# Kernel tuning notes

Measured on AMD Instinct MI355X. Metric: run time of the kernel, lower is better.

Reference implementation:

```python
import jax, jax.numpy as jnp
import numpy as np

N_NODES = 100000
N_EDGES = 1_600_000
IN_DIM, HID, OUT_DIM, N_BLOCKS = 963, 192, 3, 6


def spmm(src, dst, w, x):
    # sparse adj @ x, adj[dst, src] = w  (COO edge list)
    msgs = x[src] * w[:, None]                      # [E, F]
    return jax.ops.segment_sum(msgs, dst, num_segments=N_NODES)


def gconv(x, src, dst, ew, w, lw, b):
    # Pixel2Mesh GConv: adj @ (x @ W) + x @ W_loop + b
    return spmm(src, dst, ew, x @ w) + x @ lw + b


def setup_inputs() -> dict:
    key = jax.random.key(0)
    ks = jax.random.split(key, 13)
    s = 0.02  # small init scale to keep deep stack numerically tame
    return {
        "inputs": jax.random.normal(ks[0], (N_NODES, IN_DIM), jnp.float32),
        "edge_src": jax.random.randint(ks[1], (N_EDGES,), 0, N_NODES),
        "edge_dst": jax.random.randint(ks[2], (N_EDGES,), 0, N_NODES),
        "edge_weight": jax.random.uniform(ks[3], (N_EDGES,), jnp.float32) / 16.0,
        "w_in": jax.random.normal(ks[4], (IN_DIM, HID), jnp.float32) * s,
        "loop_in": jax.random.normal(ks[5], (IN_DIM, HID), jnp.float32) * s,
        "b_in": jnp.zeros((HID,), jnp.float32),
        "blocks_w": jax.random.normal(ks[6], (N_BLOCKS, 2, HID, HID), jnp.float32) * s,
        "blocks_loop": jax.random.normal(ks[7], (N_BLOCKS, 2, HID, HID), jnp.float32) * s,
        "blocks_b": jnp.zeros((N_BLOCKS, 2, HID), jnp.float32),
        "w_out": jax.random.normal(ks[8], (HID, OUT_DIM), jnp.float32) * s,
        "loop_out": jax.random.normal(ks[9], (HID, OUT_DIM), jnp.float32) * s,
        "b_out": jnp.zeros((OUT_DIM,), jnp.float32),
    }


def reference(inputs, edge_src, edge_dst, edge_weight, w_in, loop_in, b_in,
              blocks_w, blocks_loop, blocks_b, w_out, loop_out, b_out):
    x = gconv(inputs, edge_src, edge_dst, edge_weight, w_in, loop_in, b_in)

    def block(x, params):
        bw, bl, bb = params
        h = gconv(x, edge_src, edge_dst, edge_weight, bw[0], bl[0], bb[0])
        h = gconv(h, edge_src, edge_dst, edge_weight, bw[1], bl[1], bb[1])
        return (x + h) * 0.5, None

    x_cat, _ = jax.lax.scan(block, x, (blocks_w, blocks_loop, blocks_b))
    x_out = gconv(x_cat, edge_src, edge_dst, edge_weight, w_out, loop_out, b_out)
    return (x_out, x_cat)
```

## Files before the change

### kernel.cpp

```cpp
#include <hip/hip_runtime.h>
#include <cstdint>
#include <cstddef>

#define N_NODES 100000
#define N_EDGES 1600000
#define IN_DIM 963
#define HID 192
#define OUT_DIM 3

typedef _Float16 f16x8 __attribute__((ext_vector_type(8)));
typedef float f32x4 __attribute__((ext_vector_type(4)));

__global__ void count_kernel(const int* __restrict__ dst, int* __restrict__ counts, int E) {
    int i = blockIdx.x * blockDim.x + threadIdx.x;
    if (i < E) atomicAdd(&counts[dst[i]], 1);
}

__global__ __launch_bounds__(256)
void scan_local(const int* __restrict__ counts, int* __restrict__ rp,
                int* __restrict__ bsum, int n) {
    __shared__ int sm[256];
    const int base = blockIdx.x * 1024;
    const int t = threadIdx.x;
    const int i0 = base + t * 4;
    int v[4];
#pragma unroll
    for (int j = 0; j < 4; ++j) v[j] = (i0 + j < n) ? counts[i0 + j] : 0;
    v[1] += v[0]; v[2] += v[1]; v[3] += v[2];
    sm[t] = v[3];
    __syncthreads();
    for (int off = 1; off < 256; off <<= 1) {
        int add = (t >= off) ? sm[t - off] : 0;
        __syncthreads();
        sm[t] += add;
        __syncthreads();
    }
    const int pre = (t > 0) ? sm[t - 1] : 0;
#pragma unroll
    for (int j = 0; j < 4; ++j) {
        int idx = i0 + j;
        if (idx < n) rp[idx + 1] = pre + v[j];
    }
    if (t == 255) bsum[blockIdx.x] = sm[255];
}

__global__ __launch_bounds__(128)
void scan_block(int* __restrict__ bsum, int nb) {
    __shared__ int sm[128];
    const int t = threadIdx.x;
    const int v = (t < nb) ? bsum[t] : 0;
    sm[t] = v;
    __syncthreads();
    for (int off = 1; off < 128; off <<= 1) {
        int add = (t >= off) ? sm[t - off] : 0;
        __syncthreads();
        sm[t] += add;
        __syncthreads();
    }
    if (t < nb) bsum[t] = sm[t] - v;
}

__global__ void scan_add(const int* __restrict__ bsum, int* __restrict__ rp, int n) {
    int i = blockIdx.x * blockDim.x + threadIdx.x;
    if (i < n) rp[i + 1] += bsum[i >> 10];
    if (i == 0) rp[0] = 0;
}

__global__ void copy_cursor_kernel(const int* __restrict__ rp, int* __restrict__ cursor, int n) {
    int i = blockIdx.x * blockDim.x + threadIdx.x;
    if (i < n) cursor[i] = rp[i];
}

__global__ void scatter_kernel(const int* __restrict__ src, const int* __restrict__ dst,
                               const float* __restrict__ w, int* __restrict__ cursor,
                               int* __restrict__ csr_src, float* __restrict__ csr_w,
                               int* __restrict__ csr_eid, int E) {
    int i = blockIdx.x * blockDim.x + threadIdx.x;
    if (i < E) {
        int d = dst[i];
        int p = atomicAdd(&cursor[d], 1);
        csr_src[p] = src[i];
        csr_w[p] = w[i];
        csr_eid[p] = i;
    }
}

__global__ void sortrow_kernel(const int* __restrict__ rp, int* __restrict__ csr_src,
                               float* __restrict__ csr_w, int* __restrict__ csr_eid, int n) {
    int r = blockIdx.x * blockDim.x + threadIdx.x;
    if (r >= n) return;
    int s = rp[r], e = rp[r + 1];
    for (int i = s + 1; i < e; ++i) {
        int ke = csr_eid[i]; int ks = csr_src[i]; float kw = csr_w[i];
        int j = i - 1;
        while (j >= s && csr_eid[j] > ke) {
            csr_eid[j + 1] = csr_eid[j];
            csr_src[j + 1] = csr_src[j];
            csr_w[j + 1] = csr_w[j];
            --j;
        }
        csr_eid[j + 1] = ke; csr_src[j + 1] = ks; csr_w[j + 1] = kw;
    }
}

__global__ __launch_bounds__(256)
void trans_split(const float* __restrict__ W, const float* __restrict__ L,
                 int K, int Kp, _Float16* __restrict__ out_hi, _Float16* __restrict__ out_lo) {
    __shared__ float tile[32][33];
    const int n0 = blockIdx.x * 32, k0 = blockIdx.y * 32;
    const int tx = threadIdx.x, ty = threadIdx.y;
#pragma unroll
    for (int i = 0; i < 4; ++i) {
        int k = k0 + ty + i * 8;
        int n = n0 + tx;
        float v = 0.f;
        if (k < K) v = (n < HID) ? W[(size_t)k * HID + n] : L[(size_t)k * HID + (n - HID)];
        tile[ty + i * 8][tx] = v;
    }
    __syncthreads();
#pragma unroll
    for (int i = 0; i < 4; ++i) {
        int nl = ty + i * 8;
        int n = n0 + nl;
        int k = k0 + tx;
        float v = tile[tx][nl];
        _Float16 hi = (_Float16)v;
        _Float16 lo = (_Float16)(v - (float)hi);
        out_hi[(size_t)n * Kp + k] = hi;
        out_lo[(size_t)n * Kp + k] = lo;
    }
}

__global__ __launch_bounds__(256, 2)
void gemm_lds(const float* __restrict__ X, int M, int Kx, int Kp,
              const _Float16* __restrict__ Wth, const _Float16* __restrict__ Wtl,
              const float* __restrict__ bias, const float* __restrict__ res,
              float* __restrict__ Hdst, float* __restrict__ Tdst) {
    __shared__ __align__(16) char smem[81920];

    const int m0 = blockIdx.x * 128;
    const int tid = threadIdx.x;
    const int lane = tid & 63;
    const int wave = tid >> 6;
    const int wr = wave >> 1;
    const int wc = wave & 1;
    const int kg = lane >> 4;
    const int bcol = blockIdx.y * 192;

    auto stage = [&](int k0, int cb) {
#pragma unroll
        for (int i = 0; i < 4; ++i) {
            const int id = i * 256 + tid;
            const int row = id >> 3, slot = id & 7;
            int gr = m0 + row; if (gr >= M) gr = 0;
            const int srck = k0 + ((slot ^ (row & 7)) << 2);
            const float* src = X + (size_t)gr * Kx + srck;
            void* dst = (void*)(smem + cb + (i * 256 + wave * 64) * 16);
            __builtin_amdgcn_global_load_lds(
                (const __attribute__((address_space(1))) void*)src,
                (__attribute__((address_space(3))) void*)dst, 16, 0, 0);
        }
#pragma unroll
        for (int i = 0; i < 3; ++i) {
            const int id = i * 256 + tid;
            const int row = id >> 2, slot = id & 3;
            const int srck = k0 + ((slot ^ ((row >> 1) & 3)) << 3);
            const size_t go = (size_t)(bcol + row) * Kp + srck;
            void* dsth = (void*)(smem + cb + 16384 + (i * 256 + wave * 64) * 16);
            void* dstl = (void*)(smem + cb + 28672 + (i * 256 + wave * 64) * 16);
            __builtin_amdgcn_global_load_lds(
                (const __attribute__((address_space(1))) void*)(Wth + go),
                (__attribute__((address_space(3))) void*)dsth, 16, 0, 0);
            __builtin_amdgcn_global_load_lds(
                (const __attribute__((address_space(1))) void*)(Wtl + go),
                (__attribute__((address_space(3))) void*)dstl, 16, 0, 0);
        }
    };

    f32x4 acc[4][6];
#pragma unroll
    for (int i = 0; i < 4; ++i)
#pragma unroll
        for (int j = 0; j < 6; ++j)
            acc[i][j] = f32x4{0.f, 0.f, 0.f, 0.f};

    const int nsteps = (Kx + 31) / 32;

    stage(0, 0);
    __syncthreads();

    for (int s = 0; s < nsteps; ++s) {
        const int cb = (s & 1) * 40960;
        if (s + 1 < nsteps) stage((s + 1) * 32, ((s + 1) & 1) * 40960);

        const char* cur = smem + cb;
        f16x8 fah[4], fal[4];
#pragma unroll
        for (int mi = 0; mi < 4; ++mi) {
            const int row = wr * 64 + mi * 16 + (lane & 15);
            const char* rb = cur + row * 128;
            f32x4 a0 = *(const f32x4*)(rb + ((((2 * kg)     ^ (row & 7))) << 4));
            f32x4 a1 = *(const f32x4*)(rb + ((((2 * kg + 1) ^ (row & 7))) << 4));
            f16x8 hi, lo;
#pragma unroll
            for (int j = 0; j < 4; ++j) {
                float x0 = a0[j], x1 = a1[j];
                _Float16 h0 = (_Float16)x0, h1 = (_Float16)x1;
                hi[j] = h0;     hi[4 + j] = h1;
                lo[j] = (_Float16)(x0 - (float)h0);
                lo[4 + j] = (_Float16)(x1 - (float)h1);
            }
            fah[mi] = hi; fal[mi] = lo;
        }
#pragma unroll
        for (int ni = 0; ni < 6; ++ni) {
            const int idx = wc * 96 + ni * 16 + (lane & 15);
            const int off = 16384 + idx * 64 + ((kg ^ ((idx >> 1) & 3)) << 4);
            const f16x8 fbh = *(const f16x8*)(cur + off);
            const f16x8 fbl = *(const f16x8*)(cur + off + 12288);
#pragma unroll
            for (int mi = 0; mi < 4; ++mi)
                acc[mi][ni] = __builtin_amdgcn_mfma_f32_16x16x32_f16(fah[mi], fbh, acc[mi][ni], 0, 0, 0);
#pragma unroll
            for (int mi = 0; mi < 4; ++mi)
                acc[mi][ni] = __builtin_amdgcn_mfma_f32_16x16x32_f16(fal[mi], fbh, acc[mi][ni], 0, 0, 0);
#pragma unroll
            for (int mi = 0; mi < 4; ++mi)
                acc[mi][ni] = __builtin_amdgcn_mfma_f32_16x16x32_f16(fah[mi], fbl, acc[mi][ni], 0, 0, 0);
        }
        __syncthreads();
    }

    const bool isH = (bcol == 0);
#pragma unroll
    for (int mi = 0; mi < 4; ++mi) {
        const int rbase = m0 + wr * 64 + mi * 16 + ((lane >> 4) << 2);
#pragma unroll
        for (int ni = 0; ni < 6; ++ni) {
            const int gc = wc * 96 + ni * 16 + (lane & 15);
            f32x4 v = acc[mi][ni];
            if (isH) {
#pragma unroll
                for (int j = 0; j < 4; ++j) {
                    const int row = rbase + j;
                    if (row < M) Hdst[(size_t)row * HID + gc] = v[j];
                }
            } else {
                const float bv = bias[gc];
#pragma unroll
                for (int j = 0; j < 4; ++j) {
                    const int row = rbase + j;
                    if (row < M) {
                        float t = v[j] + bv;
                        if (res != nullptr) t += res[(size_t)row * HID + gc];
                        Tdst[(size_t)row * HID + gc] = t;
                    }
                }
            }
        }
    }
}

__global__ __launch_bounds__(256, 4)
void spmm_kernel(const int* __restrict__ rp, const int* __restrict__ csrc,
                 const float* __restrict__ cw, const float* __restrict__ Hm,
                 float* __restrict__ out, float scale) {
    const int lane = threadIdx.x & 63;
    const int nwaves = (gridDim.x * blockDim.x) >> 6;
    const int ntasks = N_NODES * 3;
    for (int task = (blockIdx.x * blockDim.x + threadIdx.x) >> 6; task < ntasks;
         task += nwaves) {
        const int wid = task / 3;
        const int ch = task - wid * 3;
        const int s = __builtin_amdgcn_readfirstlane(rp[wid]);
        const int e = __builtin_amdgcn_readfirstlane(rp[wid + 1]);
        const int fo = ch * 64 + lane;
        float a = 0.f;
        int i = s;
        for (; i + 15 < e; i += 16) {
            float w[16], x[16];
#pragma unroll
            for (int u = 0; u < 16; ++u) {
                w[u] = cw[i + u];
                x[u] = Hm[(size_t)csrc[i + u] * HID + fo];
            }
#pragma unroll
            for (int u = 0; u < 16; ++u) a += w[u] * x[u];
        }
        for (; i + 3 < e; i += 4) {
            float w[4], x[4];
#pragma unroll
            for (int u = 0; u < 4; ++u) {
                w[u] = cw[i + u];
                x[u] = Hm[(size_t)csrc[i + u] * HID + fo];
            }
#pragma unroll
            for (int u = 0; u < 4; ++u) a += w[u] * x[u];
        }
        for (; i < e; ++i)
            a += cw[i] * Hm[(size_t)csrc[i] * HID + fo];
        float* o = out + (size_t)wid * HID + ch * 64;
        o[lane] = scale * (o[lane] + a);
    }
}

__global__ __launch_bounds__(256)
void out_gemm(const float* __restrict__ X, const float* __restrict__ Wout,
              const float* __restrict__ Lout, const float* __restrict__ bout,
              float* __restrict__ H3, float* __restrict__ T3) {
    __shared__ float Ws[HID * OUT_DIM];
    __shared__ float Ls[HID * OUT_DIM];
    int tid = threadIdx.x;
    for (int i = tid; i < HID * OUT_DIM; i += 256) { Ws[i] = Wout[i]; Ls[i] = Lout[i]; }
    __syncthreads();
    int n = blockIdx.x * 4 + (tid >> 6);
    int lane = tid & 63;
    if (n >= N_NODES) return;
    const float* x = X + (size_t)n * HID;
    float aw[3] = {0.f, 0.f, 0.f}, al[3] = {0.f, 0.f, 0.f};
#pragma unroll
    for (int p = 0; p < 3; ++p) {
        int k = p * 64 + lane;
        float xv = x[k];
#pragma unroll
        for (int c = 0; c < 3; ++c) {
            aw[c] += xv * Ws[k * 3 + c];
            al[c] += xv * Ls[k * 3 + c];
        }
    }
#pragma unroll
    for (int off = 32; off > 0; off >>= 1) {
#pragma unroll
        for (int c = 0; c < 3; ++c) {
            aw[c] += __shfl_down(aw[c], off, 64);
            al[c] += __shfl_down(al[c], off, 64);
        }
    }
    if (lane == 0) {
#pragma unroll
        for (int c = 0; c < 3; ++c) {
            H3[n * 3 + c] = aw[c];
            T3[n * 3 + c] = al[c] + bout[c];
        }
    }
}

__global__ __launch_bounds__(256)
void out_spmm(const int* __restrict__ rp, const int* __restrict__ csrc,
              const float* __restrict__ cw, const float* __restrict__ H3,
              const float* __restrict__ T3, float* __restrict__ out) {
    int n = blockIdx.x * blockDim.x + threadIdx.x;
    if (n >= N_NODES) return;
    int s = rp[n], e = rp[n + 1];
    float a0 = 0.f, a1 = 0.f, a2 = 0.f;
    for (int i = s; i < e; ++i) {
        float w = cw[i];
        int src = csrc[i];
        a0 += w * H3[src * 3 + 0];
        a1 += w * H3[src * 3 + 1];
        a2 += w * H3[src * 3 + 2];
    }
    out[n * 3 + 0] = a0 + T3[n * 3 + 0];
    out[n * 3 + 1] = a1 + T3[n * 3 + 1];
    out[n * 3 + 2] = a2 + T3[n * 3 + 2];
}

extern "C" void kernel_launch(void* const* d_in, const int* in_sizes, int n_in,
                              void* d_out, int out_size, void* d_ws, size_t ws_size,
                              hipStream_t stream) {
    const float* X0    = (const float*)d_in[0];
    const int*   esrc  = (const int*)d_in[1];
    const int*   edst  = (const int*)d_in[2];
    const float* ew    = (const float*)d_in[3];
    const float* w_in  = (const float*)d_in[4];
    const float* l_in  = (const float*)d_in[5];
    const float* b_in  = (const float*)d_in[6];
    const float* bw    = (const float*)d_in[7];
    const float* bl    = (const float*)d_in[8];
    const float* bb    = (const float*)d_in[9];
    const float* w_out = (const float*)d_in[10];
    const float* l_out = (const float*)d_in[11];
    const float* b_out = (const float*)d_in[12];

    char* ws = (char*)d_ws;
    size_t off = 0;
    auto alloc = [&](size_t bytes) -> void* {
        void* p = ws + off;
        off += (bytes + 255) & ~(size_t)255;
        return p;
    };
    float* Hbuf   = (float*)alloc(sizeof(float) * (size_t)N_NODES * HID);
    float* h1     = (float*)alloc(sizeof(float) * (size_t)N_NODES * HID);
    int*   counts = (int*)alloc(sizeof(int) * N_NODES);
    int*   rp     = (int*)alloc(sizeof(int) * (N_NODES + 1));
    int*   cursor = (int*)alloc(sizeof(int) * N_NODES);
    int*   bsum   = (int*)alloc(sizeof(int) * 128);
    int*   csrc   = (int*)alloc(sizeof(int) * N_EDGES);
    float* cw     = (float*)alloc(sizeof(float) * N_EDGES);
    int*   ceid   = (int*)alloc(sizeof(int) * N_EDGES);
    float* H3     = (float*)alloc(sizeof(float) * (size_t)N_NODES * OUT_DIM);
    float* T3     = (float*)alloc(sizeof(float) * (size_t)N_NODES * OUT_DIM);
    const int KP0 = 992;
    _Float16* Wt0h = (_Float16*)alloc(sizeof(_Float16) * 384 * KP0);
    _Float16* Wt0l = (_Float16*)alloc(sizeof(_Float16) * 384 * KP0);
    _Float16* WtHh = (_Float16*)alloc(sizeof(_Float16) * 12 * 384 * HID);
    _Float16* WtHl = (_Float16*)alloc(sizeof(_Float16) * 12 * 384 * HID);

    float* xout = (float*)d_out;
    float* xcat = (float*)d_out + (size_t)N_NODES * OUT_DIM;

    trans_split<<<dim3(12, 31), dim3(32, 8), 0, stream>>>(w_in, l_in, IN_DIM, KP0, Wt0h, Wt0l);
    for (int l = 0; l < 12; ++l) {
        trans_split<<<dim3(12, 6), dim3(32, 8), 0, stream>>>(
            bw + (size_t)l * HID * HID, bl + (size_t)l * HID * HID, HID, HID,
            WtHh + (size_t)l * 384 * HID, WtHl + (size_t)l * 384 * HID);
    }

    const int NB = (N_NODES + 1023) / 1024;
    hipMemsetAsync(counts, 0, sizeof(int) * N_NODES, stream);
    count_kernel<<<(N_EDGES + 255) / 256, 256, 0, stream>>>(edst, counts, N_EDGES);
    scan_local<<<NB, 256, 0, stream>>>(counts, rp, bsum, N_NODES);
    scan_block<<<1, 128, 0, stream>>>(bsum, NB);
    scan_add<<<(N_NODES + 255) / 256, 256, 0, stream>>>(bsum, rp, N_NODES);
    copy_cursor_kernel<<<(N_NODES + 255) / 256, 256, 0, stream>>>(rp, cursor, N_NODES);
    scatter_kernel<<<(N_EDGES + 255) / 256, 256, 0, stream>>>(esrc, edst, ew, cursor,
                                                              csrc, cw, ceid, N_EDGES);
    sortrow_kernel<<<(N_NODES + 255) / 256, 256, 0, stream>>>(rp, csrc, cw, ceid, N_NODES);

    const dim3 gemm_grid((N_NODES + 127) / 128, 2);
    const int spmm_blocks = 1024;

    gemm_lds<<<gemm_grid, 256, 0, stream>>>(X0, N_NODES, IN_DIM, KP0, Wt0h, Wt0l,
                                            b_in, nullptr, Hbuf, xcat);
    spmm_kernel<<<spmm_blocks, 256, 0, stream>>>(rp, csrc, cw, Hbuf, xcat, 1.0f);

    for (int b = 0; b < 6; ++b) {
        int l0 = b * 2, l1 = b * 2 + 1;
        const float* B0 = bb + (size_t)l0 * HID;
        const float* B1 = bb + (size_t)l1 * HID;

        gemm_lds<<<gemm_grid, 256, 0, stream>>>(xcat, N_NODES, HID, HID,
                                                WtHh + (size_t)l0 * 384 * HID,
                                                WtHl + (size_t)l0 * 384 * HID,
                                                B0, nullptr, Hbuf, h1);
        spmm_kernel<<<spmm_blocks, 256, 0, stream>>>(rp, csrc, cw, Hbuf, h1, 1.0f);
        gemm_lds<<<gemm_grid, 256, 0, stream>>>(h1, N_NODES, HID, HID,
                                                WtHh + (size_t)l1 * 384 * HID,
                                                WtHl + (size_t)l1 * 384 * HID,
                                                B1, xcat, Hbuf, xcat);
        spmm_kernel<<<spmm_blocks, 256, 0, stream>>>(rp, csrc, cw, Hbuf, xcat, 0.5f);
    }

    out_gemm<<<(N_NODES + 3) / 4, 256, 0, stream>>>(xcat, w_out, l_out, b_out, H3, T3);
    out_spmm<<<(N_NODES + 255) / 256, 256, 0, stream>>>(rp, csrc, cw, H3, T3, xout);
}
```

Measured before the change: 4.628 ms.

## Vectorize SpMM with one wave per row and batch weight transposes

The SpMM kernel now assigns one wave per destination row instead of three waves per row, and 48 lanes each load float4 feature slices, so the edge index and weight loads are amortized across all 192 features. The unroll changes from 16 to 8 and the SpMM grid size doubles. The twelve per-layer weight transpose launches are merged into a single 3D-grid launch. In exchange, 16 lanes per wave sit idle and each lane holds more registers.

```diff
diff --git a/kernel.cpp b/kernel.cpp
--- a/kernel.cpp
+++ b/kernel.cpp
@@ -103,11 +103,11 @@
     }
 }
 
-__global__ __launch_bounds__(256)
-void trans_split(const float* __restrict__ W, const float* __restrict__ L,
-                 int K, int Kp, _Float16* __restrict__ out_hi, _Float16* __restrict__ out_lo) {
+__device__ __forceinline__ void trans_split_body(
+        const float* W, const float* L, int K, int Kp,
+        _Float16* out_hi, _Float16* out_lo, int bx, int by) {
     __shared__ float tile[32][33];
-    const int n0 = blockIdx.x * 32, k0 = blockIdx.y * 32;
+    const int n0 = bx * 32, k0 = by * 32;
     const int tx = threadIdx.x, ty = threadIdx.y;
 #pragma unroll
     for (int i = 0; i < 4; ++i) {
@@ -129,6 +129,21 @@
         out_hi[(size_t)n * Kp + k] = hi;
         out_lo[(size_t)n * Kp + k] = lo;
     }
+}
+
+__global__ __launch_bounds__(256)
+void trans_split(const float* __restrict__ W, const float* __restrict__ L,
+                 int K, int Kp, _Float16* __restrict__ out_hi, _Float16* __restrict__ out_lo) {
+    trans_split_body(W, L, K, Kp, out_hi, out_lo, blockIdx.x, blockIdx.y);
+}
+
+__global__ __launch_bounds__(256)
+void trans_split_all(const float* __restrict__ bw, const float* __restrict__ bl,
+                     _Float16* __restrict__ outh, _Float16* __restrict__ outl) {
+    const int l = blockIdx.z;
+    trans_split_body(bw + (size_t)l * HID * HID, bl + (size_t)l * HID * HID, HID, HID,
+                     outh + (size_t)l * 384 * HID, outl + (size_t)l * 384 * HID,
+                     blockIdx.x, blockIdx.y);
 }
 
 __global__ __launch_bounds__(256, 2)
@@ -266,41 +281,49 @@
                  const float* __restrict__ cw, const float* __restrict__ Hm,
                  float* __restrict__ out, float scale) {
     const int lane = threadIdx.x & 63;
+    const bool act = lane < 48;
+    const int fo = act ? lane * 4 : 0;
     const int nwaves = (gridDim.x * blockDim.x) >> 6;
-    const int ntasks = N_NODES * 3;
-    for (int task = (blockIdx.x * blockDim.x + threadIdx.x) >> 6; task < ntasks;
-         task += nwaves) {
-        const int wid = task / 3;
-        const int ch = task - wid * 3;
+    for (int wid = (blockIdx.x * blockDim.x + threadIdx.x) >> 6; wid < N_NODES;
+         wid += nwaves) {
         const int s = __builtin_amdgcn_readfirstlane(rp[wid]);
         const int e = __builtin_amdgcn_readfirstlane(rp[wid + 1]);
-        const int fo = ch * 64 + lane;
-        float a = 0.f;
+        f32x4 a = {0.f, 0.f, 0.f, 0.f};
         int i = s;
-        for (; i + 15 < e; i += 16) {
-            float w[16], x[16];
-#pragma unroll
-            for (int u = 0; u < 16; ++u) {
+        for (; i + 7 < e; i += 8) {
+            float w[8];
+            f32x4 x[8];
+#pragma unroll
+            for (int u = 0; u < 8; ++u) {
                 w[u] = cw[i + u];
-                x[u] = Hm[(size_t)csrc[i + u] * HID + fo];
+                x[u] = *(const f32x4*)(Hm + (size_t)csrc[i + u] * HID + fo);
             }
 #pragma unroll
-            for (int u = 0; u < 16; ++u) a += w[u] * x[u];
-        }
-        for (; i + 3 < e; i += 4) {
-            float w[4], x[4];
-#pragma unroll
-            for (int u = 0; u < 4; ++u) {
-                w[u] = cw[i + u];
-                x[u] = Hm[(size_t)csrc[i + u] * HID + fo];
+            for (int u = 0; u < 8; ++u) {
+                a[0] += w[u] * x[u][0];
+                a[1] += w[u] * x[u][1];
+                a[2] += w[u] * x[u][2];
+                a[3] += w[u] * x[u][3];
             }
-#pragma unroll
-            for (int u = 0; u < 4; ++u) a += w[u] * x[u];
-        }
-        for (; i < e; ++i)
-            a += cw[i] * Hm[(size_t)csrc[i] * HID + fo];
-        float* o = out + (size_t)wid * HID + ch * 64;
-        o[lane] = scale * (o[lane] + a);
+        }
+        for (; i < e; ++i) {
+            const float w = cw[i];
+            const f32x4 x = *(const f32x4*)(Hm + (size_t)csrc[i] * HID + fo);
+            a[0] += w * x[0];
+            a[1] += w * x[1];
+            a[2] += w * x[2];
+            a[3] += w * x[3];
+        }
+        if (act) {
+            float* o = out + (size_t)wid * HID + fo;
+            f32x4 ov = *(const f32x4*)o;
+            f32x4 r;
+            r[0] = scale * (ov[0] + a[0]);
+            r[1] = scale * (ov[1] + a[1]);
+            r[2] = scale * (ov[2] + a[2]);
+            r[3] = scale * (ov[3] + a[3]);
+            *(f32x4*)o = r;
+        }
     }
 }
 
@@ -410,11 +433,7 @@
     float* xcat = (float*)d_out + (size_t)N_NODES * OUT_DIM;
 
     trans_split<<<dim3(12, 31), dim3(32, 8), 0, stream>>>(w_in, l_in, IN_DIM, KP0, Wt0h, Wt0l);
-    for (int l = 0; l < 12; ++l) {
-        trans_split<<<dim3(12, 6), dim3(32, 8), 0, stream>>>(
-            bw + (size_t)l * HID * HID, bl + (size_t)l * HID * HID, HID, HID,
-            WtHh + (size_t)l * 384 * HID, WtHl + (size_t)l * 384 * HID);
-    }
+    trans_split_all<<<dim3(12, 6, 12), dim3(32, 8), 0, stream>>>(bw, bl, WtHh, WtHl);
 
     const int NB = (N_NODES + 1023) / 1024;
     hipMemsetAsync(counts, 0, sizeof(int) * N_NODES, stream);
@@ -428,7 +447,7 @@
     sortrow_kernel<<<(N_NODES + 255) / 256, 256, 0, stream>>>(rp, csrc, cw, ceid, N_NODES);
 
     const dim3 gemm_grid((N_NODES + 127) / 128, 2);
-    const int spmm_blocks = 1024;
+    const int spmm_blocks = 2048;
 
     gemm_lds<<<gemm_grid, 256, 0, stream>>>(X0, N_NODES, IN_DIM, KP0, Wt0h, Wt0l,
                                             b_in, nullptr, Hbuf, xcat);
```

Result: no change. 4.541 ms (-1.9%).
